# Kernel tuning notes

Measured on AMD Instinct MI355X. Metric: run time of the kernel, lower is better.

The kernel has to match this reference:

```python
import jax, jax.numpy as jnp
import numpy as np


def _rope(x, fr, fi):
    # Faithful port of apply_rotary_embeddings: deinterleave even/odd elements,
    # reshape to (-1, *fr.shape), rotate, then concat halves and reshape back.
    shp = x.shape
    dims = fr.shape  # (seq_len, 1, head_dim//2)
    xf = x.reshape(-1, 2)
    xr = xf[:, 0].reshape((-1,) + dims)
    xi = xf[:, 1].reshape((-1,) + dims)
    out_r = xr * fr - xi * fi
    out_i = xr * fi + xi * fr
    return jnp.concatenate([out_r, out_i], axis=-1).reshape(shp).astype(x.dtype)


def setup_inputs() -> dict:
    key = jax.random.key(0)
    ks = jax.random.split(key, 9)
    B, S, Dm, H, Hd, P = 16, 1, 4096, 32, 128, 2048
    W = 0.02  # weight scale to keep score magnitudes sane
    return {
        "x": jax.random.normal(ks[0], (B, S, Dm), jnp.float32),
        "cache_k": jax.random.normal(ks[1], (B, P, H, Hd), jnp.float32),
        "cache_v": jax.random.normal(ks[2], (B, P, H, Hd), jnp.float32),
        "freqs_real": jax.random.normal(ks[3], (S, 1, Hd // 2), jnp.float32),
        "freqs_imag": jax.random.normal(ks[4], (S, 1, Hd // 2), jnp.float32),
        "dwq": jax.random.normal(ks[5], (Dm, Dm), jnp.float32) * W,
        "dwk": jax.random.normal(ks[6], (Dm, Dm), jnp.float32) * W,
        "dwv": jax.random.normal(ks[7], (Dm, Dm), jnp.float32) * W,
        "dwo": jax.random.normal(ks[8], (Dm, Dm), jnp.float32) * W,
        "start_pos": P,
    }


def reference(x, cache_k, cache_v, freqs_real, freqs_imag, dwq, dwk, dwv, dwo, start_pos):
    B, S, _ = x.shape
    H, Hd = cache_k.shape[2], cache_k.shape[3]
    scale = 1.0 / np.float32(np.sqrt(Hd))

    xq = (x @ dwq.T).reshape(B, S, H, Hd)
    xk = (x @ dwk.T).reshape(B, S, H, Hd)
    xv = (x @ dwv.T).reshape(B, S, H, Hd)
    xq = _rope(xq, freqs_real, freqs_imag)
    xk = _rope(xk, freqs_real, freqs_imag)

    # KV-cache append (cat-based growth in the original)
    keys = jnp.concatenate([cache_k, xk], axis=1)      # (B, P+S, H, Hd)
    values = jnp.concatenate([cache_v, xv], axis=1)

    q = xq.transpose(0, 2, 1, 3)       # (B, H, S, Hd)
    k = keys.transpose(0, 2, 1, 3)     # (B, H, P+S, Hd)
    v = values.transpose(0, 2, 1, 3)

    scores = jnp.einsum('bhqd,bhkd->bhqk', q, k) * scale
    probs = jax.nn.softmax(scores.astype(jnp.float32), axis=-1).astype(q.dtype)
    out = jnp.einsum('bhqk,bhkd->bhqd', probs, v)
    out = out.transpose(0, 2, 1, 3).reshape(B, S, H * Hd)
    return out @ dwo.T  # allreduce is identity with tp=1
```

## Files before the change

kernel.cpp:

```cpp
#include <hip/hip_runtime.h>
#include <cstdint>

#define DM 4096
#define NB 16
#define NH 32
#define HD 128
#define PP 2048
#define NCHUNK 32
#define CROWS 64
#define PSTRIDE 132

typedef __attribute__((ext_vector_type(8))) short bf16x8;
typedef __attribute__((ext_vector_type(4))) float f32x4;

__device__ inline float bf2f(short s) {
  return __uint_as_float(((uint32_t)(uint16_t)s) << 16);
}
__device__ inline f32x4 ntld4(const float* p) {
  return __builtin_nontemporal_load(reinterpret_cast<const f32x4*>(p));
}

__device__ inline void split_pair(float x0, float x1, uint32_t& hpair,
                                  uint32_t& lpair) {
  uint32_t u0 = __float_as_uint(x0), u1 = __float_as_uint(x1);
  hpair = __builtin_amdgcn_perm(u1, u0, 0x07060302u);
  float l0 = x0 - __uint_as_float(u0 & 0xFFFF0000u);
  float l1 = x1 - __uint_as_float(u1 & 0xFFFF0000u);
  asm("v_cvt_pk_bf16_f32 %0, %1, %2" : "=v"(lpair) : "v"(l0), "v"(l1));
}

template <int NW, bool ROPE>
__device__ inline void gemv16(const float* __restrict__ A,
                              const float* __restrict__ W,
                              float* __restrict__ O, int jt,
                              const float* __restrict__ fr,
                              const float* __restrict__ fi) {
  const int wave = threadIdx.x >> 6;
  const int lane = threadIdx.x & 63;
  const int m = lane & 15;
  const int kg = lane >> 4;
  const float* arow = A + (size_t)m * DM;
  const float* wrow = W + (size_t)(jt + m) * DM;
  const int kbase = wave * (DM / NW) + kg * 8;
  f32x4 acc = {0.f, 0.f, 0.f, 0.f};
#pragma unroll 2
  for (int kb = 0; kb < (DM / NW) / 32; ++kb) {
    const int k = kbase + kb * 32;
    f32x4 xa = *(const f32x4*)(arow + k);
    f32x4 xb = *(const f32x4*)(arow + k + 4);
    f32x4 wa = ntld4(wrow + k);
    f32x4 wb = ntld4(wrow + k + 4);
    union { bf16x8 v; uint32_t d[4]; } ah, al, wh, wl;
    split_pair(xa.x, xa.y, ah.d[0], al.d[0]);
    split_pair(xa.z, xa.w, ah.d[1], al.d[1]);
    split_pair(xb.x, xb.y, ah.d[2], al.d[2]);
    split_pair(xb.z, xb.w, ah.d[3], al.d[3]);
    split_pair(wa.x, wa.y, wh.d[0], wl.d[0]);
    split_pair(wa.z, wa.w, wh.d[1], wl.d[1]);
    split_pair(wb.x, wb.y, wh.d[2], wl.d[2]);
    split_pair(wb.z, wb.w, wh.d[3], wl.d[3]);
    acc = __builtin_amdgcn_mfma_f32_16x16x32_bf16(ah.v, wh.v, acc, 0, 0, 0);
    acc = __builtin_amdgcn_mfma_f32_16x16x32_bf16(ah.v, wl.v, acc, 0, 0, 0);
    acc = __builtin_amdgcn_mfma_f32_16x16x32_bf16(al.v, wh.v, acc, 0, 0, 0);
  }
  __shared__ float red[NW][256];
  red[wave][lane * 4 + 0] = acc[0];
  red[wave][lane * 4 + 1] = acc[1];
  red[wave][lane * 4 + 2] = acc[2];
  red[wave][lane * 4 + 3] = acc[3];
  __syncthreads();
  const int t = threadIdx.x;
  float s = 0.f;
  if (t < 256) {
#pragma unroll
    for (int w = 0; w < NW; ++w) s += red[w][t];
  }
  float part = 0.f;
  if (ROPE) {
    __syncthreads();
    if (t < 256) red[0][t] = s;
    __syncthreads();
    if (t < 256) part = red[0][t ^ 4];
  }
  if (t < 256) {
    const int l = t >> 2, r = t & 3;
    const int bb = ((l >> 4) << 2) + r;
    const int n = l & 15;
    const int c = jt + n;
    float val;
    int oc;
    if (ROPE) {
      const int j = (c & 127) >> 1;
      const float f_r = fr[j], f_i = fi[j];
      if ((c & 1) == 0) {
        val = s * f_r - part * f_i;
        oc = (c & ~127) + j;
      } else {
        val = part * f_i + s * f_r;
        oc = (c & ~127) + 64 + j;
      }
    } else {
      val = s;
      oc = c;
    }
    O[(size_t)bb * DM + oc] = val;
  }
}

__global__ __launch_bounds__(256) void qkv_proj_kernel(
    const float* __restrict__ x, const float* __restrict__ wq,
    const float* __restrict__ wk, const float* __restrict__ wv,
    const float* __restrict__ fr, const float* __restrict__ fi,
    float* __restrict__ oq, float* __restrict__ ok, float* __restrict__ ov) {
  const int g = blockIdx.x >> 8;
  const int jt = (blockIdx.x & 255) << 4;
  if (g == 0)
    gemv16<4, true>(x, wq, oq, jt, fr, fi);
  else if (g == 1)
    gemv16<4, true>(x, wk, ok, jt, fr, fi);
  else
    gemv16<4, false>(x, wv, ov, jt, nullptr, nullptr);
}

__global__ __launch_bounds__(1024, 4) void oproj_kernel(
    const float* __restrict__ a, const float* __restrict__ w,
    float* __restrict__ o) {
  gemv16<16, false>(a, w, o, blockIdx.x << 4, nullptr, nullptr);
}

__global__ __launch_bounds__(512) void attn_chunk_kernel(
    const float* __restrict__ qrope, const float* __restrict__ cache_k,
    const float* __restrict__ cache_v, float* __restrict__ part) {
  const int b = blockIdx.x >> 5;
  const int c = blockIdx.x & 31;
  const int t = threadIdx.x;
  __shared__ float sc[NH][CROWS];

  const f32x4 qa = *(const f32x4*)(qrope + (size_t)b * DM + 4 * t);
  const f32x4 qb = *(const f32x4*)(qrope + (size_t)b * DM + 2048 + 4 * t);
  const int h1 = t >> 5;
  const int h2 = h1 + 16;
  const float scale = 0.08838834764831845f;

  const float* Kb = cache_k + ((size_t)b * PP + (size_t)c * CROWS) * DM;
#pragma unroll 2
  for (int r = 0; r < CROWS; ++r) {
    const float* krow = Kb + (size_t)r * DM + 4 * t;
    f32x4 k1 = ntld4(krow);
    f32x4 k2 = ntld4(krow + 2048);
    float p1 = qa.x * k1.x + qa.y * k1.y + qa.z * k1.z + qa.w * k1.w;
    float p2 = qb.x * k2.x + qb.y * k2.y + qb.z * k2.z + qb.w * k2.w;
#pragma unroll
    for (int off = 1; off <= 16; off <<= 1) {
      p1 += __shfl_xor(p1, off);
      p2 += __shfl_xor(p2, off);
    }
    if ((t & 31) == 0) {
      sc[h1][r] = p1 * scale;
      sc[h2][r] = p2 * scale;
    }
  }
  __syncthreads();

  const int hh = t >> 4, u = t & 15;
  float4 sv4 = *(const float4*)(&sc[hh][u * 4]);
  float mx = fmaxf(fmaxf(sv4.x, sv4.y), fmaxf(sv4.z, sv4.w));
#pragma unroll
  for (int off = 1; off <= 8; off <<= 1) mx = fmaxf(mx, __shfl_xor(mx, off));
  float e0 = __expf(sv4.x - mx), e1 = __expf(sv4.y - mx);
  float e2 = __expf(sv4.z - mx), e3 = __expf(sv4.w - mx);
  float4 ev = {e0, e1, e2, e3};
  *(float4*)(&sc[hh][u * 4]) = ev;
  float sm = (e0 + e1) + (e2 + e3);
#pragma unroll
  for (int off = 1; off <= 8; off <<= 1) sm += __shfl_xor(sm, off);
  float* pb = part + ((size_t)(b * NCHUNK + c) * NH) * PSTRIDE;
  if (u == 0) {
    pb[hh * PSTRIDE + 128] = mx;
    pb[hh * PSTRIDE + 129] = sm;
  }
  __syncthreads();

  const float* Vb = cache_v + ((size_t)b * PP + (size_t)c * CROWS) * DM;
  f32x4 a1 = {0.f, 0.f, 0.f, 0.f}, a2 = {0.f, 0.f, 0.f, 0.f};
#pragma unroll 2
  for (int r = 0; r < CROWS; ++r) {
    const float* vrow = Vb + (size_t)r * DM + 4 * t;
    f32x4 v1 = ntld4(vrow);
    f32x4 v2 = ntld4(vrow + 2048);
    float w1 = sc[h1][r], w2 = sc[h2][r];
    a1 += w1 * v1;
    a2 += w2 * v2;
  }
  const int dbase = (4 * t) & 127;
  *(f32x4*)(pb + h1 * PSTRIDE + dbase) = a1;
  *(f32x4*)(pb + h2 * PSTRIDE + dbase) = a2;
}

__global__ __launch_bounds__(128) void attn_combine_kernel(
    const float* __restrict__ qrope, const float* __restrict__ krope,
    const float* __restrict__ vraw, const float* __restrict__ part,
    float* __restrict__ aout) {
  const int b = blockIdx.x >> 5;
  const int h = blockIdx.x & 31;
  const int d = threadIdx.x;
  __shared__ float red2[2];
  __shared__ float mv[NCHUNK], sv[NCHUNK], ec[NCHUNK];
  const size_t qoff = (size_t)b * DM + h * HD + d;
  float p = qrope[qoff] * krope[qoff];
#pragma unroll
  for (int off = 1; off <= 32; off <<= 1) p += __shfl_xor(p, off);
  if ((d & 63) == 0) red2[d >> 6] = p;
  const float* pb = part + ((size_t)b * NCHUNK * NH + h) * PSTRIDE;
  if (d < NCHUNK) {
    mv[d] = pb[(size_t)d * NH * PSTRIDE + 128];
    sv[d] = pb[(size_t)d * NH * PSTRIDE + 129];
  }
  __syncthreads();
  const float scale = 0.08838834764831845f;
  const float snew = (red2[0] + red2[1]) * scale;
  float M = snew;
#pragma unroll
  for (int c = 0; c < NCHUNK; ++c) M = fmaxf(M, mv[c]);
  if (d < NCHUNK) ec[d] = __expf(mv[d] - M);
  __syncthreads();
  const float en = __expf(snew - M);
  float S = en;
  float acc = en * vraw[qoff];
#pragma unroll 4
  for (int c = 0; c < NCHUNK; ++c) {
    acc += ec[c] * pb[(size_t)c * NH * PSTRIDE + d];
    S += ec[c] * sv[c];
  }
  aout[qoff] = acc / S;
}

extern "C" void kernel_launch(void* const* d_in, const int* in_sizes, int n_in,
                              void* d_out, int out_size, void* d_ws, size_t ws_size,
                              hipStream_t stream) {
  const float* x = (const float*)d_in[0];
  const float* cache_k = (const float*)d_in[1];
  const float* cache_v = (const float*)d_in[2];
  const float* fr = (const float*)d_in[3];
  const float* fi = (const float*)d_in[4];
  const float* dwq = (const float*)d_in[5];
  const float* dwk = (const float*)d_in[6];
  const float* dwv = (const float*)d_in[7];
  const float* dwo = (const float*)d_in[8];
  float* out = (float*)d_out;

  float* qrope = (float*)d_ws;
  float* krope = qrope + NB * DM;
  float* vraw = krope + NB * DM;
  float* aout = vraw + NB * DM;
  float* part = aout + NB * DM;

  qkv_proj_kernel<<<768, 256, 0, stream>>>(x, dwq, dwk, dwv, fr, fi,
                                           qrope, krope, vraw);
  attn_chunk_kernel<<<512, 512, 0, stream>>>(qrope, cache_k, cache_v, part);
  attn_combine_kernel<<<512, 128, 0, stream>>>(qrope, krope, vraw, part, aout);
  oproj_kernel<<<256, 1024, 0, stream>>>(aout, dwo, out);
}
```

Before: 240.9 us.

## Stage weight rows through double-buffered LDS panels with coalesced loads in GEMV

The GEMV now loads 16 weight rows as 256-wide K panels into a double-buffered shared-memory tile with fully coalesced row-contiguous loads, and prefetches the next panel while MFMAs run on the current one. Previously each lane read 32-byte pieces scattered across 16 rows directly from global memory. The o-projection kernel drops from 1024 to 256 threads to share the same 4-wave path. This adds a block barrier per panel and leaves fewer waves in flight for the o-projection, which is bandwidth bound.

```diff
diff --git a/kernel.cpp b/kernel.cpp
--- a/kernel.cpp
+++ b/kernel.cpp
@@ -9,13 +9,12 @@
 #define NCHUNK 32
 #define CROWS 64
 #define PSTRIDE 132
+#define KP 256
+#define NPAN (DM / KP)
 
 typedef __attribute__((ext_vector_type(8))) short bf16x8;
 typedef __attribute__((ext_vector_type(4))) float f32x4;
 
-__device__ inline float bf2f(short s) {
-  return __uint_as_float(((uint32_t)(uint16_t)s) << 16);
-}
 __device__ inline f32x4 ntld4(const float* p) {
   return __builtin_nontemporal_load(reinterpret_cast<const f32x4*>(p));
 }
@@ -29,7 +28,7 @@
   asm("v_cvt_pk_bf16_f32 %0, %1, %2" : "=v"(lpair) : "v"(l0), "v"(l1));
 }
 
-template <int NW, bool ROPE>
+template <bool ROPE>
 __device__ inline void gemv16(const float* __restrict__ A,
                               const float* __restrict__ W,
                               float* __restrict__ O, int jt,
@@ -40,71 +39,103 @@
   const int m = lane & 15;
   const int kg = lane >> 4;
   const float* arow = A + (size_t)m * DM;
-  const float* wrow = W + (size_t)(jt + m) * DM;
-  const int kbase = wave * (DM / NW) + kg * 8;
+
+  __shared__ float wt[2][16][KP + 4];
+  __shared__ float red[4][256];
+
   f32x4 acc = {0.f, 0.f, 0.f, 0.f};
-#pragma unroll 2
-  for (int kb = 0; kb < (DM / NW) / 32; ++kb) {
-    const int k = kbase + kb * 32;
-    f32x4 xa = *(const f32x4*)(arow + k);
-    f32x4 xb = *(const f32x4*)(arow + k + 4);
-    f32x4 wa = ntld4(wrow + k);
-    f32x4 wb = ntld4(wrow + k + 4);
-    union { bf16x8 v; uint32_t d[4]; } ah, al, wh, wl;
-    split_pair(xa.x, xa.y, ah.d[0], al.d[0]);
-    split_pair(xa.z, xa.w, ah.d[1], al.d[1]);
-    split_pair(xb.x, xb.y, ah.d[2], al.d[2]);
-    split_pair(xb.z, xb.w, ah.d[3], al.d[3]);
-    split_pair(wa.x, wa.y, wh.d[0], wl.d[0]);
-    split_pair(wa.z, wa.w, wh.d[1], wl.d[1]);
-    split_pair(wb.x, wb.y, wh.d[2], wl.d[2]);
-    split_pair(wb.z, wb.w, wh.d[3], wl.d[3]);
-    acc = __builtin_amdgcn_mfma_f32_16x16x32_bf16(ah.v, wh.v, acc, 0, 0, 0);
-    acc = __builtin_amdgcn_mfma_f32_16x16x32_bf16(ah.v, wl.v, acc, 0, 0, 0);
-    acc = __builtin_amdgcn_mfma_f32_16x16x32_bf16(al.v, wh.v, acc, 0, 0, 0);
-  }
-  __shared__ float red[NW][256];
+
+  {
+    f32x4 s0[4];
+#pragma unroll
+    for (int j = 0; j < 4; ++j) {
+      const int row = wave * 4 + j;
+      s0[j] = ntld4(W + (size_t)(jt + row) * DM + lane * 4);
+    }
+#pragma unroll
+    for (int j = 0; j < 4; ++j) {
+      const int row = wave * 4 + j;
+      *(f32x4*)&wt[0][row][lane * 4] = s0[j];
+    }
+  }
+  __syncthreads();
+
+  int buf = 0;
+  for (int p = 0; p < NPAN; ++p) {
+    f32x4 stg[4];
+    if (p + 1 < NPAN) {
+#pragma unroll
+      for (int j = 0; j < 4; ++j) {
+        const int row = wave * 4 + j;
+        stg[j] = ntld4(W + (size_t)(jt + row) * DM + (p + 1) * KP + lane * 4);
+      }
+    }
+#pragma unroll
+    for (int s = 0; s < 2; ++s) {
+      const int kl = (wave << 6) + (s << 5) + kg * 8;
+      f32x4 wa = *(const f32x4*)&wt[buf][m][kl];
+      f32x4 wb = *(const f32x4*)&wt[buf][m][kl + 4];
+      f32x4 xa = *(const f32x4*)(arow + p * KP + kl);
+      f32x4 xb = *(const f32x4*)(arow + p * KP + kl + 4);
+      union { bf16x8 v; uint32_t d[4]; } ah, al, wh, wl;
+      split_pair(xa.x, xa.y, ah.d[0], al.d[0]);
+      split_pair(xa.z, xa.w, ah.d[1], al.d[1]);
+      split_pair(xb.x, xb.y, ah.d[2], al.d[2]);
+      split_pair(xb.z, xb.w, ah.d[3], al.d[3]);
+      split_pair(wa.x, wa.y, wh.d[0], wl.d[0]);
+      split_pair(wa.z, wa.w, wh.d[1], wl.d[1]);
+      split_pair(wb.x, wb.y, wh.d[2], wl.d[2]);
+      split_pair(wb.z, wb.w, wh.d[3], wl.d[3]);
+      acc = __builtin_amdgcn_mfma_f32_16x16x32_bf16(ah.v, wh.v, acc, 0, 0, 0);
+      acc = __builtin_amdgcn_mfma_f32_16x16x32_bf16(ah.v, wl.v, acc, 0, 0, 0);
+      acc = __builtin_amdgcn_mfma_f32_16x16x32_bf16(al.v, wh.v, acc, 0, 0, 0);
+    }
+    if (p + 1 < NPAN) {
+#pragma unroll
+      for (int j = 0; j < 4; ++j) {
+        const int row = wave * 4 + j;
+        *(f32x4*)&wt[buf ^ 1][row][lane * 4] = stg[j];
+      }
+    }
+    __syncthreads();
+    buf ^= 1;
+  }
+
   red[wave][lane * 4 + 0] = acc[0];
   red[wave][lane * 4 + 1] = acc[1];
   red[wave][lane * 4 + 2] = acc[2];
   red[wave][lane * 4 + 3] = acc[3];
   __syncthreads();
   const int t = threadIdx.x;
-  float s = 0.f;
-  if (t < 256) {
-#pragma unroll
-    for (int w = 0; w < NW; ++w) s += red[w][t];
-  }
+  float s = red[0][t] + red[1][t] + red[2][t] + red[3][t];
   float part = 0.f;
   if (ROPE) {
     __syncthreads();
-    if (t < 256) red[0][t] = s;
+    red[0][t] = s;
     __syncthreads();
-    if (t < 256) part = red[0][t ^ 4];
-  }
-  if (t < 256) {
-    const int l = t >> 2, r = t & 3;
-    const int bb = ((l >> 4) << 2) + r;
-    const int n = l & 15;
-    const int c = jt + n;
-    float val;
-    int oc;
-    if (ROPE) {
-      const int j = (c & 127) >> 1;
-      const float f_r = fr[j], f_i = fi[j];
-      if ((c & 1) == 0) {
-        val = s * f_r - part * f_i;
-        oc = (c & ~127) + j;
-      } else {
-        val = part * f_i + s * f_r;
-        oc = (c & ~127) + 64 + j;
-      }
+    part = red[0][t ^ 4];
+  }
+  const int l = t >> 2, r = t & 3;
+  const int bb = ((l >> 4) << 2) + r;
+  const int n = l & 15;
+  const int c = jt + n;
+  float val;
+  int oc;
+  if (ROPE) {
+    const int j = (c & 127) >> 1;
+    const float f_r = fr[j], f_i = fi[j];
+    if ((c & 1) == 0) {
+      val = s * f_r - part * f_i;
+      oc = (c & ~127) + j;
     } else {
-      val = s;
-      oc = c;
-    }
-    O[(size_t)bb * DM + oc] = val;
-  }
+      val = part * f_i + s * f_r;
+      oc = (c & ~127) + 64 + j;
+    }
+  } else {
+    val = s;
+    oc = c;
+  }
+  O[(size_t)bb * DM + oc] = val;
 }
 
 __global__ __launch_bounds__(256) void qkv_proj_kernel(
@@ -115,17 +146,17 @@
   const int g = blockIdx.x >> 8;
   const int jt = (blockIdx.x & 255) << 4;
   if (g == 0)
-    gemv16<4, true>(x, wq, oq, jt, fr, fi);
+    gemv16<true>(x, wq, oq, jt, fr, fi);
   else if (g == 1)
-    gemv16<4, true>(x, wk, ok, jt, fr, fi);
+    gemv16<true>(x, wk, ok, jt, fr, fi);
   else
-    gemv16<4, false>(x, wv, ov, jt, nullptr, nullptr);
-}
-
-__global__ __launch_bounds__(1024, 4) void oproj_kernel(
+    gemv16<false>(x, wv, ov, jt, nullptr, nullptr);
+}
+
+__global__ __launch_bounds__(256) void oproj_kernel(
     const float* __restrict__ a, const float* __restrict__ w,
     float* __restrict__ o) {
-  gemv16<16, false>(a, w, o, blockIdx.x << 4, nullptr, nullptr);
+  gemv16<false>(a, w, o, blockIdx.x << 4, nullptr, nullptr);
 }
 
 __global__ __launch_bounds__(512) void attn_chunk_kernel(
@@ -259,5 +290,5 @@
                                            qrope, krope, vraw);
   attn_chunk_kernel<<<512, 512, 0, stream>>>(qrope, cache_k, cache_v, part);
   attn_combine_kernel<<<512, 128, 0, stream>>>(qrope, krope, vraw, part, aout);
-  oproj_kernel<<<256, 1024, 0, stream>>>(aout, dwo, out);
-}
+  oproj_kernel<<<256, 256, 0, stream>>>(aout, dwo, out);
+}
```

Measured after the change: 241.4 us. No clear change (+0.2%).
